# Performance work log

Hardware: AMD Instinct MI355X
Metric: run time of the kernel (lower is better)

The kernel has to match this reference:

```python
import jax, jax.numpy as jnp
import numpy as np

# ---- static config (mirrors init_kwargs + fixed setup box dims) ----
PC_MIN = jnp.array([0.0, -40.0, -3.0])
VOXEL_SIZE = jnp.array([0.05, 0.05, 0.1])
STRIDE = 4                     # pool_cfg.STRIDE and multi_scale_3d_strides['x_conv4']
EXTEND = 2.0                   # model_cfg.ROI_EXTEND_FACTOR
GRID_ZYX = (10, 400, 352)      # sparse spatial shape after stride-4 downsample [z,y,x]
# grid_size = round(extended_dims / voxel_size / STRIDE) for fixed dims [6.4,3.2,1.6]
GX, GY, GZ = 64, 32, 4
G = GX * GY * GZ
N_VOX, C = 200_000, 128
M = 64
KX, KY, KZ = 7, 7, 3


def setup_inputs() -> dict:
    key = jax.random.key(0)
    k1, k2, k3, k4, k5, k6, k7, k8, k9 = jax.random.split(key, 9)
    ctr = jnp.stack([
        jax.random.uniform(k1, (M,), minval=10.0, maxval=60.0),
        jax.random.uniform(k2, (M,), minval=-25.0, maxval=25.0),
        jax.random.uniform(k3, (M,), minval=-1.5, maxval=0.5)], axis=-1)
    dims = jnp.tile(jnp.array([[6.4, 3.2, 1.6]], jnp.float32), (M, 1))  # fixed -> static grid
    yaw = jax.random.uniform(k4, (M, 1), minval=-np.pi, maxval=np.pi)
    rois = jnp.concatenate([ctr, dims, yaw], axis=-1).astype(jnp.float32)
    proto_box = jnp.array([0.0, 0.0, 0.0, 6.4, 3.2, 1.6, 0.3], jnp.float32)
    voxel_feats = jax.random.normal(k5, (N_VOX, C), jnp.float32)
    feat_proto = jax.random.normal(k6, (1, KX, KY, KZ, C), jnp.float32) * 0.1
    zc = jax.random.randint(k7, (N_VOX,), 0, GRID_ZYX[0])
    yc = jax.random.randint(k8, (N_VOX,), 0, GRID_ZYX[1])
    xc = jax.random.randint(k9, (N_VOX,), 0, GRID_ZYX[2])
    voxel_coords = jnp.stack([jnp.zeros_like(zc), zc, yc, xc], -1).astype(jnp.int32)
    return dict(rois=rois, proto_box=proto_box, voxel_feats=voxel_feats,
                feat_proto=feat_proto, voxel_coords=voxel_coords)


def _dense_grid_points(box):
    # get_dense_grid_points: row-major (x,y,z) index order, matches torch nonzero()
    idx = jnp.stack(jnp.meshgrid(jnp.arange(GX), jnp.arange(GY), jnp.arange(GZ),
                                 indexing='ij'), -1).reshape(-1, 3).astype(jnp.float32)
    gs = jnp.array([GX, GY, GZ], jnp.float32)
    return (idx + 0.5) / gs * box[3:6] - box[3:6] / 2.0  # (G,3)


def _rotate_z(pts, ang):
    # common_utils.rotate_points_along_z: pts @ [[c,s,0],[-s,c,0],[0,0,1]]
    c, s = jnp.cos(ang), jnp.sin(ang)
    R = jnp.stack([jnp.stack([c, s, 0.0 * c]),
                   jnp.stack([-s, c, 0.0 * c]),
                   jnp.stack([0.0 * c, 0.0 * c, 1.0 + 0.0 * c])])
    return pts @ R


def reference(rois, proto_box, voxel_feats, feat_proto, voxel_coords):
    # generate_voxel2pinds: dense [Z,Y,X] grid of voxel row indices, -1 = empty
    v2p = -jnp.ones(GRID_ZYX, jnp.int32)
    v2p = v2p.at[voxel_coords[:, 1], voxel_coords[:, 2], voxel_coords[:, 3]].set(
        jnp.arange(N_VOX, dtype=jnp.int32))

    def per_roi(box):
        box = box.at[3:5].multiply(EXTEND)                 # xy_dim_extend
        local = _dense_grid_points(box)                    # (G,3)
        xyz = _rotate_z(local, box[6]) + box[:3]           # global roi grid points
        coords = jnp.floor((xyz - PC_MIN) / VOXEL_SIZE)    # '//' floor-div semantics
        coords = jnp.floor(coords / STRIDE).astype(jnp.int32)
        xc, yc, zc = coords[:, 0], coords[:, 1], coords[:, 2]
        inb = ((zc >= 0) & (zc < GRID_ZYX[0]) & (yc >= 0) & (yc < GRID_ZYX[1]) &
               (xc >= 0) & (xc < GRID_ZYX[2]))
        pidx = v2p[jnp.clip(zc, 0, GRID_ZYX[0] - 1),
                   jnp.clip(yc, 0, GRID_ZYX[1] - 1),
                   jnp.clip(xc, 0, GRID_ZYX[2] - 1)]
        valid = inb & (pidx >= 0)
        feat = jnp.where(valid[:, None], voxel_feats[jnp.clip(pidx, 0)], 0.0)  # (G,C)
        return feat, xyz

    feats, grid_xyz = jax.vmap(per_roi)(rois)              # (M,G,C), (M,G,3)
    vol = feats.reshape(M, GX, GY, GZ, C).transpose(0, 4, 1, 2, 3)   # NCDHW
    kern = feat_proto.transpose(0, 4, 1, 2, 3)                        # (1,C,KX,KY,KZ)
    pads = [(KX // 2,) * 2, (KY // 2,) * 2, (KZ // 2,) * 2]           # ceil((k-1)/2)
    mm = jax.lax.conv_general_dilated(vol, kern, (1, 1, 1), pads,
                                      dimension_numbers=('NCDHW', 'OIDHW', 'NCDHW'))
    # fresh BatchNorm3d(1) applied per-ROI (batch 1 each call): per-sample norm
    mu = jnp.mean(mm, axis=(1, 2, 3, 4), keepdims=True)
    var = jnp.var(mm, axis=(1, 2, 3, 4), keepdims=True)
    mm = (mm - mu) / jnp.sqrt(var + 1e-5)
    idx = jnp.minimum(jnp.argmax(mm.reshape(M, -1), axis=1), G - 1)
    sel = jnp.take_along_axis(grid_xyz, idx[:, None, None], axis=1)[:, 0, :]  # (M,3)
    rois_new = jnp.tile(proto_box[None], (M, 1))
    rois_new = rois_new.at[:, :3].set(sel)
    return rois_new
```

## Files before the change

### kernel.cpp

```cpp
#include <hip/hip_runtime.h>
#include <stdint.h>

#define GRID_Z 10
#define GRID_Y 400
#define GRID_X 352
#define NGRID (GRID_Z * GRID_Y * GRID_X)
#define NVOX 200000
#define CCH 128
#define MROI 64
#define GXD 64
#define GYD 32
#define GZD 4
#define GCELLS 8192
#define NTAPS 147
#define FPAD 132
#define TROWS 32

__device__ __forceinline__ void cell_xyz(const float* __restrict__ roi, int g,
                                         float& X, float& Y, float& Z) {
#pragma clang fp contract(off)
    int iz = g & 3;
    int iy = (g >> 2) & 31;
    int ix = g >> 7;
    float bx = roi[3] * 2.0f;
    float by = roi[4] * 2.0f;
    float bz = roi[5];
    float lx = (ix + 0.5f) / 64.0f * bx - bx / 2.0f;
    float ly = (iy + 0.5f) / 32.0f * by - by / 2.0f;
    float lz = (iz + 0.5f) / 4.0f  * bz - bz / 2.0f;
    float c = cosf(roi[6]);
    float s = sinf(roi[6]);
    X = lx * c + ly * (-s) + roi[0];
    Y = lx * s + ly * c    + roi[1];
    Z = lz + roi[2];
}

__global__ void k_scatter(const int* __restrict__ vcoords, int* __restrict__ v2p,
                          int* __restrict__ cnt) {
    int i = blockIdx.x * 256 + threadIdx.x;
    if (blockIdx.x == 0 && threadIdx.x < MROI) cnt[threadIdx.x] = 0;
    if (i >= NVOX) return;
    int z = vcoords[i * 4 + 1];
    int y = vcoords[i * 4 + 2];
    int x = vcoords[i * 4 + 3];
    atomicMax(&v2p[(z * GRID_Y + y) * GRID_X + x], i);
}

__global__ void k_build(const float* __restrict__ rois, const int* __restrict__ v2p,
                        unsigned* __restrict__ list, int* __restrict__ cnt) {
#pragma clang fp contract(off)
    int g = blockIdx.x * 256 + threadIdx.x;
    int m = blockIdx.y;
    int lane = threadIdx.x & 63;
    const float* roi = rois + m * 7;
    float X, Y, Z;
    cell_xyz(roi, g, X, Y, Z);
    float fx = floorf((X - 0.0f)     / 0.05f);
    float fy = floorf((Y - (-40.0f)) / 0.05f);
    float fz = floorf((Z - (-3.0f))  / 0.1f);
    int cx = (int)floorf(fx / 4.0f);
    int cy = (int)floorf(fy / 4.0f);
    int cz = (int)floorf(fz / 4.0f);
    int p = -1;
    if (cz >= 0 && cz < GRID_Z && cy >= 0 && cy < GRID_Y && cx >= 0 && cx < GRID_X)
        p = v2p[(cz * GRID_Y + cy) * GRID_X + cx];
    bool v = p >= 0;
    unsigned long long bal = __ballot(v);
    int nset = __popcll(bal);
    int base = 0;
    if (lane == 0 && nset) base = atomicAdd(&cnt[m], nset);
    base = __shfl(base, 0, 64);
    if (v) {
        int pos = __popcll(bal & ((1ull << lane) - 1ull));
        list[m * GCELLS + base + pos] = ((unsigned)p << 13) | (unsigned)g;
    }
}

__global__ __launch_bounds__(256) void k_dots(
        const float* __restrict__ vfeat, const float* __restrict__ fproto,
        const unsigned* __restrict__ list, const int* __restrict__ cnt,
        float* __restrict__ partial) {
    __shared__ float    sscore[GCELLS];
    __shared__ float    sfeat[TROWS * FPAD];
    __shared__ unsigned sg[TROWS];

    const int m    = blockIdx.y;
    const int NS   = gridDim.x;
    const int tid  = threadIdx.x;
    const int w    = tid >> 6;
    const int lane = tid & 63;
    const int vi   = lane & 7;
    const int ti   = (lane >> 3) & 7;
    const int n    = cnt[m];
    const unsigned* lst = list + m * GCELLS;
    const int tbase = w * 40 + ti;

    int tkx[5], tky[5], tkz[5], tok[5];
    #pragma unroll
    for (int b = 0; b < 5; ++b) {
        int t = tbase + 8 * b;
        tok[b] = t < NTAPS;
        int tc = tok[b] ? t : (NTAPS - 1);
        int kx  = tc / 21;
        int rem = tc - kx * 21;
        tkx[b] = kx;
        tky[b] = rem / 3;
        tkz[b] = rem - tky[b] * 3;
    }

    {
        float4* s4 = (float4*)sscore;
        #pragma unroll
        for (int i = 0; i < GCELLS / 4 / 256; ++i)
            s4[tid + 256 * i] = make_float4(0.f, 0.f, 0.f, 0.f);
    }

    for (int vt0 = blockIdx.x * TROWS; vt0 < n; vt0 += TROWS * NS) {
        __syncthreads();
        {
            int r = tid >> 3;
            int q = tid & 7;
            int v = vt0 + r;
            unsigned e = 0xFFFFFFFFu;
            if (v < n) e = lst[v];
            if (q == 0) sg[r] = e;
            if (e != 0xFFFFFFFFu) {
                int p = (int)(e >> 13);
                const float4* src = (const float4*)(vfeat + (size_t)p * CCH) + q * 4;
                float4* drow = (float4*)(sfeat + r * FPAD + q * 16);
                #pragma unroll
                for (int j = 0; j < 4; ++j) drow[j] = src[j];
            }
        }
        __syncthreads();

        float acc[4][5];
        #pragma unroll
        for (int a = 0; a < 4; ++a)
            #pragma unroll
            for (int b = 0; b < 5; ++b) acc[a][b] = 0.0f;

        #pragma unroll 1
        for (int k = 0; k < CCH; k += 4) {
            float4 f[4];
            #pragma unroll
            for (int a = 0; a < 4; ++a)
                f[a] = *(const float4*)&sfeat[(vi + 8 * a) * FPAD + k];
            float4 wv[5];
            #pragma unroll
            for (int b = 0; b < 5; ++b)
                wv[b] = *(const float4*)(fproto + (tbase + (tok[b] ? 8 * b : 0)) * CCH + k);
            #pragma unroll
            for (int a = 0; a < 4; ++a)
                #pragma unroll
                for (int b = 0; b < 5; ++b) {
                    acc[a][b] = fmaf(f[a].x, wv[b].x, acc[a][b]);
                    acc[a][b] = fmaf(f[a].y, wv[b].y, acc[a][b]);
                    acc[a][b] = fmaf(f[a].z, wv[b].z, acc[a][b]);
                    acc[a][b] = fmaf(f[a].w, wv[b].w, acc[a][b]);
                }
        }

        #pragma unroll
        for (int b = 0; b < 5; ++b) {
            if (!tok[b]) continue;
            #pragma unroll
            for (int a = 0; a < 4; ++a) {
                unsigned e = sg[vi + 8 * a];
                if (e == 0xFFFFFFFFu) continue;
                int g  = (int)(e & 8191u);
                int cx = (g >> 7)        - (tkx[b] - 3);
                int cy = ((g >> 2) & 31) - (tky[b] - 3);
                int cz = (g & 3)         - (tkz[b] - 1);
                if ((unsigned)cx < (unsigned)GXD && (unsigned)cy < (unsigned)GYD &&
                    (unsigned)cz < (unsigned)GZD)
                    atomicAdd(&sscore[(cx << 7) | (cy << 2) | cz], acc[a][b]);
            }
        }
    }

    __syncthreads();
    {
        float* dst = partial + ((size_t)m * NS + blockIdx.x) * GCELLS;
        const float4* s4 = (const float4*)sscore;
        float4* d4 = (float4*)dst;
        #pragma unroll
        for (int i = 0; i < GCELLS / 4 / 256; ++i)
            d4[tid + 256 * i] = s4[tid + 256 * i];
    }
}

template <int NS>
__global__ __launch_bounds__(1024) void k_argfin(
        const float* __restrict__ partial,
        const float* __restrict__ rois,
        const float* __restrict__ pbox,
        float* __restrict__ out) {
    __shared__ unsigned long long red[1024];
    int m = blockIdx.x;
    int tid = threadIdx.x;
    const float* base = partial + (size_t)m * NS * GCELLS;
    unsigned long long bk = 0ull;
    #pragma unroll
    for (int i = 0; i < GCELLS / 1024; ++i) {
        int g = tid + 1024 * i;
        float v = 0.0f;
        #pragma unroll
        for (int s = 0; s < NS; ++s) v += base[s * GCELLS + g];
        unsigned ub  = __float_as_uint(v);
        unsigned key = (ub & 0x80000000u) ? ~ub : (ub | 0x80000000u);
        unsigned long long pk =
            ((unsigned long long)key << 32) | (unsigned)(GCELLS - 1 - g);
        bk = bk > pk ? bk : pk;
    }
    red[tid] = bk;
    __syncthreads();
    for (int s = 512; s > 0; s >>= 1) {
        if (tid < s) {
            unsigned long long o = red[tid + s];
            if (o > red[tid]) red[tid] = o;
        }
        __syncthreads();
    }
    if (tid == 0) {
        int g = (GCELLS - 1) - (int)(unsigned)(red[0] & 0xFFFFFFFFu);
        float X, Y, Z;
        cell_xyz(rois + m * 7, g, X, Y, Z);
        out[m * 7 + 0] = X;
        out[m * 7 + 1] = Y;
        out[m * 7 + 2] = Z;
        out[m * 7 + 3] = pbox[3];
        out[m * 7 + 4] = pbox[4];
        out[m * 7 + 5] = pbox[5];
        out[m * 7 + 6] = pbox[6];
    }
}

extern "C" void kernel_launch(void* const* d_in, const int* in_sizes, int n_in,
                              void* d_out, int out_size, void* d_ws, size_t ws_size,
                              hipStream_t stream) {
    const float* rois    = (const float*)d_in[0];
    const float* pbox    = (const float*)d_in[1];
    const float* vfeat   = (const float*)d_in[2];
    const float* fproto  = (const float*)d_in[3];
    const int*   vcoords = (const int*)d_in[4];
    float* out = (float*)d_out;

    int*      v2p  = (int*)d_ws;
    unsigned* list = (unsigned*)(v2p + NGRID);
    int*      cnt  = (int*)(list + MROI * GCELLS);
    size_t    base = ((size_t)NGRID + (size_t)MROI * GCELLS) * 4 + 256;
    int NS; float* partial;
    if (ws_size >= base + (size_t)12 * MROI * GCELLS * 4) {
        NS = 12; partial = (float*)((char*)d_ws + base);
    } else if (ws_size >= base + (size_t)8 * MROI * GCELLS * 4) {
        NS = 8;  partial = (float*)((char*)d_ws + base);
    } else if (ws_size >= base + (size_t)4 * MROI * GCELLS * 4) {
        NS = 4;  partial = (float*)((char*)d_ws + base);
    } else {
        NS = 2;  partial = (float*)v2p;
    }

    hipMemsetAsync(v2p, 0xFF, (size_t)NGRID * 4, stream);
    k_scatter<<<(NVOX + 255) / 256, 256, 0, stream>>>(vcoords, v2p, cnt);
    k_build  <<<dim3(GCELLS / 256, MROI), 256, 0, stream>>>(rois, v2p, list, cnt);
    k_dots   <<<dim3(NS, MROI), 256, 0, stream>>>(vfeat, fproto, list, cnt, partial);
    if (NS == 12)      k_argfin<12><<<MROI, 1024, 0, stream>>>(partial, rois, pbox, out);
    else if (NS == 8)  k_argfin<8> <<<MROI, 1024, 0, stream>>>(partial, rois, pbox, out);
    else if (NS == 4)  k_argfin<4> <<<MROI, 1024, 0, stream>>>(partial, rois, pbox, out);
    else               k_argfin<2> <<<MROI, 1024, 0, stream>>>(partial, rois, pbox, out);
}
```

Baseline: 300.5 us.

## Fuse pipeline into one cooperative kernel with grid syncs

Replaces the memset plus four separate kernel launches with a single cooperative kernel that runs the v2p reset, scatter, list build, dot-product scoring and argmax phases, separated by grid-wide barriers. The argmax is split across all 768 blocks, each reducing a chunk and combining through a 64-bit atomicMax. The aim is to remove launch gaps and the tail of the small argmax kernel. In exchange, the phases now cost grid.sync overhead, and the 768 blocks must all be resident (the code requires at least 3 blocks per CU, each using about 49KB of shared memory). If the occupancy check or the cooperative launch fails, it falls back to the old multi-kernel path.

```diff
diff --git a/kernel.cpp b/kernel.cpp
--- a/kernel.cpp
+++ b/kernel.cpp
@@ -1,5 +1,8 @@
 #include <hip/hip_runtime.h>
+#include <hip/hip_cooperative_groups.h>
 #include <stdint.h>
+
+namespace cg = cooperative_groups;
 
 #define GRID_Z 10
 #define GRID_Y 400
@@ -15,6 +18,10 @@
 #define NTAPS 147
 #define FPAD 132
 #define TROWS 32
+#define NS12 12
+#define NBLK (NS12 * MROI)
+#define NTH  (NBLK * 256)
+#define CHUNK ((GCELLS + NS12 - 1) / NS12)
 
 __device__ __forceinline__ void cell_xyz(const float* __restrict__ roi, int g,
                                          float& X, float& Y, float& Z) {
@@ -35,24 +42,9 @@
     Z = lz + roi[2];
 }
 
-__global__ void k_scatter(const int* __restrict__ vcoords, int* __restrict__ v2p,
-                          int* __restrict__ cnt) {
-    int i = blockIdx.x * 256 + threadIdx.x;
-    if (blockIdx.x == 0 && threadIdx.x < MROI) cnt[threadIdx.x] = 0;
-    if (i >= NVOX) return;
-    int z = vcoords[i * 4 + 1];
-    int y = vcoords[i * 4 + 2];
-    int x = vcoords[i * 4 + 3];
-    atomicMax(&v2p[(z * GRID_Y + y) * GRID_X + x], i);
-}
-
-__global__ void k_build(const float* __restrict__ rois, const int* __restrict__ v2p,
-                        unsigned* __restrict__ list, int* __restrict__ cnt) {
+__device__ __forceinline__ int cell_to_pidx(const float* __restrict__ roi, int g,
+                                            const int* __restrict__ v2p) {
 #pragma clang fp contract(off)
-    int g = blockIdx.x * 256 + threadIdx.x;
-    int m = blockIdx.y;
-    int lane = threadIdx.x & 63;
-    const float* roi = rois + m * 7;
     float X, Y, Z;
     cell_xyz(roi, g, X, Y, Z);
     float fx = floorf((X - 0.0f)     / 0.05f);
@@ -64,6 +56,224 @@
     int p = -1;
     if (cz >= 0 && cz < GRID_Z && cy >= 0 && cy < GRID_Y && cx >= 0 && cx < GRID_X)
         p = v2p[(cz * GRID_Y + cy) * GRID_X + cx];
+    return p;
+}
+
+__global__ __launch_bounds__(256) void k_mega(
+        const float* __restrict__ rois, const float* __restrict__ pbox,
+        const float* __restrict__ vfeat, const float* __restrict__ fproto,
+        const int* __restrict__ vcoords,
+        int* __restrict__ v2p, unsigned* __restrict__ list, int* __restrict__ cnt,
+        float* __restrict__ partial, unsigned long long* __restrict__ best,
+        float* __restrict__ out) {
+    __shared__ float    sscore[GCELLS];
+    __shared__ float    sfeat[TROWS * FPAD];
+    __shared__ unsigned sg[TROWS];
+
+    cg::grid_group grid = cg::this_grid();
+    const int tid  = threadIdx.x;
+    const int gtid = blockIdx.x * 256 + tid;
+    const int lane = tid & 63;
+
+    for (int i = gtid; i < NGRID; i += NTH) v2p[i] = -1;
+    if (gtid < MROI) { cnt[gtid] = 0; best[gtid] = 0ull; }
+    grid.sync();
+
+    for (int i = gtid; i < NVOX; i += NTH) {
+        int z = vcoords[i * 4 + 1];
+        int y = vcoords[i * 4 + 2];
+        int x = vcoords[i * 4 + 3];
+        atomicMax(&v2p[(z * GRID_Y + y) * GRID_X + x], i);
+    }
+    grid.sync();
+
+    for (int idx = gtid; idx < MROI * GCELLS; idx += NTH) {
+        int m = idx >> 13;
+        int g = idx & 8191;
+        int p = cell_to_pidx(rois + m * 7, g, v2p);
+        bool v = p >= 0;
+        unsigned long long bal = __ballot(v);
+        int nset = __popcll(bal);
+        int base = 0;
+        if (lane == 0 && nset) base = atomicAdd(&cnt[m], nset);
+        base = __shfl(base, 0, 64);
+        if (v) {
+            int pos = __popcll(bal & ((1ull << lane) - 1ull));
+            list[m * GCELLS + base + pos] = ((unsigned)p << 13) | (unsigned)g;
+        }
+    }
+    grid.sync();
+
+    {
+        const int m = blockIdx.x & 63;
+        const int s = blockIdx.x >> 6;
+        const int w    = tid >> 6;
+        const int vi   = lane & 7;
+        const int ti   = (lane >> 3) & 7;
+        const int n    = cnt[m];
+        const unsigned* lst = list + m * GCELLS;
+        const int tbase = w * 40 + ti;
+
+        int tkx[5], tky[5], tkz[5], tok[5];
+        #pragma unroll
+        for (int b = 0; b < 5; ++b) {
+            int t = tbase + 8 * b;
+            tok[b] = t < NTAPS;
+            int tc = tok[b] ? t : (NTAPS - 1);
+            int kx  = tc / 21;
+            int rem = tc - kx * 21;
+            tkx[b] = kx;
+            tky[b] = rem / 3;
+            tkz[b] = rem - tky[b] * 3;
+        }
+
+        {
+            float4* s4 = (float4*)sscore;
+            #pragma unroll
+            for (int i = 0; i < GCELLS / 4 / 256; ++i)
+                s4[tid + 256 * i] = make_float4(0.f, 0.f, 0.f, 0.f);
+        }
+
+        for (int vt0 = s * TROWS; vt0 < n; vt0 += TROWS * NS12) {
+            __syncthreads();
+            {
+                int r = tid >> 3;
+                int q = tid & 7;
+                int v = vt0 + r;
+                unsigned e = 0xFFFFFFFFu;
+                if (v < n) e = lst[v];
+                if (q == 0) sg[r] = e;
+                if (e != 0xFFFFFFFFu) {
+                    int p = (int)(e >> 13);
+                    const float4* src = (const float4*)(vfeat + (size_t)p * CCH) + q * 4;
+                    float4* drow = (float4*)(sfeat + r * FPAD + q * 16);
+                    #pragma unroll
+                    for (int j = 0; j < 4; ++j) drow[j] = src[j];
+                }
+            }
+            __syncthreads();
+
+            float acc[4][5];
+            #pragma unroll
+            for (int a = 0; a < 4; ++a)
+                #pragma unroll
+                for (int b = 0; b < 5; ++b) acc[a][b] = 0.0f;
+
+            #pragma unroll 1
+            for (int k = 0; k < CCH; k += 4) {
+                float4 f[4];
+                #pragma unroll
+                for (int a = 0; a < 4; ++a)
+                    f[a] = *(const float4*)&sfeat[(vi + 8 * a) * FPAD + k];
+                float4 wv[5];
+                #pragma unroll
+                for (int b = 0; b < 5; ++b)
+                    wv[b] = *(const float4*)(fproto + (tbase + (tok[b] ? 8 * b : 0)) * CCH + k);
+                #pragma unroll
+                for (int a = 0; a < 4; ++a)
+                    #pragma unroll
+                    for (int b = 0; b < 5; ++b) {
+                        acc[a][b] = fmaf(f[a].x, wv[b].x, acc[a][b]);
+                        acc[a][b] = fmaf(f[a].y, wv[b].y, acc[a][b]);
+                        acc[a][b] = fmaf(f[a].z, wv[b].z, acc[a][b]);
+                        acc[a][b] = fmaf(f[a].w, wv[b].w, acc[a][b]);
+                    }
+            }
+
+            #pragma unroll
+            for (int b = 0; b < 5; ++b) {
+                if (!tok[b]) continue;
+                #pragma unroll
+                for (int a = 0; a < 4; ++a) {
+                    unsigned e = sg[vi + 8 * a];
+                    if (e == 0xFFFFFFFFu) continue;
+                    int g  = (int)(e & 8191u);
+                    int cx = (g >> 7)        - (tkx[b] - 3);
+                    int cy = ((g >> 2) & 31) - (tky[b] - 3);
+                    int cz = (g & 3)         - (tkz[b] - 1);
+                    if ((unsigned)cx < (unsigned)GXD && (unsigned)cy < (unsigned)GYD &&
+                        (unsigned)cz < (unsigned)GZD)
+                        atomicAdd(&sscore[(cx << 7) | (cy << 2) | cz], acc[a][b]);
+                }
+            }
+        }
+
+        __syncthreads();
+        {
+            float* dst = partial + ((size_t)m * NS12 + s) * GCELLS;
+            const float4* s4 = (const float4*)sscore;
+            float4* d4 = (float4*)dst;
+            #pragma unroll
+            for (int i = 0; i < GCELLS / 4 / 256; ++i)
+                d4[tid + 256 * i] = s4[tid + 256 * i];
+        }
+    }
+    grid.sync();
+
+    {
+        int m = blockIdx.x & 63;
+        int s = blockIdx.x >> 6;
+        const float* basep = partial + (size_t)m * NS12 * GCELLS;
+        int c0 = s * CHUNK;
+        int c1 = c0 + CHUNK < GCELLS ? c0 + CHUNK : GCELLS;
+        unsigned long long bk = 0ull;
+        for (int c = c0 + tid; c < c1; c += 256) {
+            float v = 0.0f;
+            #pragma unroll
+            for (int q = 0; q < NS12; ++q) v += basep[q * GCELLS + c];
+            unsigned ub  = __float_as_uint(v);
+            unsigned key = (ub & 0x80000000u) ? ~ub : (ub | 0x80000000u);
+            unsigned long long pk =
+                ((unsigned long long)key << 32) | (unsigned)(GCELLS - 1 - c);
+            bk = bk > pk ? bk : pk;
+        }
+        __syncthreads();
+        unsigned long long* red = reinterpret_cast<unsigned long long*>(sscore);
+        red[tid] = bk;
+        __syncthreads();
+        for (int st = 128; st > 0; st >>= 1) {
+            if (tid < st) {
+                unsigned long long o = red[tid + st];
+                if (o > red[tid]) red[tid] = o;
+            }
+            __syncthreads();
+        }
+        if (tid == 0) atomicMax(&best[m], red[0]);
+    }
+    grid.sync();
+
+    if (blockIdx.x == 0 && tid < MROI) {
+        int m = tid;
+        int g = (GCELLS - 1) - (int)(unsigned)(best[m] & 0xFFFFFFFFu);
+        float X, Y, Z;
+        cell_xyz(rois + m * 7, g, X, Y, Z);
+        out[m * 7 + 0] = X;
+        out[m * 7 + 1] = Y;
+        out[m * 7 + 2] = Z;
+        out[m * 7 + 3] = pbox[3];
+        out[m * 7 + 4] = pbox[4];
+        out[m * 7 + 5] = pbox[5];
+        out[m * 7 + 6] = pbox[6];
+    }
+}
+
+__global__ void k_scatter(const int* __restrict__ vcoords, int* __restrict__ v2p,
+                          int* __restrict__ cnt) {
+    int i = blockIdx.x * 256 + threadIdx.x;
+    if (blockIdx.x == 0 && threadIdx.x < MROI) cnt[threadIdx.x] = 0;
+    if (i >= NVOX) return;
+    int z = vcoords[i * 4 + 1];
+    int y = vcoords[i * 4 + 2];
+    int x = vcoords[i * 4 + 3];
+    atomicMax(&v2p[(z * GRID_Y + y) * GRID_X + x], i);
+}
+
+__global__ void k_build(const float* __restrict__ rois, const int* __restrict__ v2p,
+                        unsigned* __restrict__ list, int* __restrict__ cnt) {
+    int g = blockIdx.x * 256 + threadIdx.x;
+    int m = blockIdx.y;
+    int lane = threadIdx.x & 63;
+    int p = cell_to_pidx(rois + m * 7, g, v2p);
     bool v = p >= 0;
     unsigned long long bal = __ballot(v);
     int nset = __popcll(bal);
@@ -85,7 +295,7 @@
     __shared__ unsigned sg[TROWS];
 
     const int m    = blockIdx.y;
-    const int NS   = gridDim.x;
+    const int NSd  = gridDim.x;
     const int tid  = threadIdx.x;
     const int w    = tid >> 6;
     const int lane = tid & 63;
@@ -103,24 +313,18 @@
         int tc = tok[b] ? t : (NTAPS - 1);
         int kx  = tc / 21;
         int rem = tc - kx * 21;
-        tkx[b] = kx;
-        tky[b] = rem / 3;
-        tkz[b] = rem - tky[b] * 3;
-    }
-
+        tkx[b] = kx; tky[b] = rem / 3; tkz[b] = rem - tky[b] * 3;
+    }
     {
         float4* s4 = (float4*)sscore;
         #pragma unroll
         for (int i = 0; i < GCELLS / 4 / 256; ++i)
             s4[tid + 256 * i] = make_float4(0.f, 0.f, 0.f, 0.f);
     }
-
-    for (int vt0 = blockIdx.x * TROWS; vt0 < n; vt0 += TROWS * NS) {
+    for (int vt0 = blockIdx.x * TROWS; vt0 < n; vt0 += TROWS * NSd) {
         __syncthreads();
         {
-            int r = tid >> 3;
-            int q = tid & 7;
-            int v = vt0 + r;
+            int r = tid >> 3, q = tid & 7, v = vt0 + r;
             unsigned e = 0xFFFFFFFFu;
             if (v < n) e = lst[v];
             if (q == 0) sg[r] = e;
@@ -133,13 +337,11 @@
             }
         }
         __syncthreads();
-
         float acc[4][5];
         #pragma unroll
         for (int a = 0; a < 4; ++a)
             #pragma unroll
             for (int b = 0; b < 5; ++b) acc[a][b] = 0.0f;
-
         #pragma unroll 1
         for (int k = 0; k < CCH; k += 4) {
             float4 f[4];
@@ -160,7 +362,6 @@
                     acc[a][b] = fmaf(f[a].w, wv[b].w, acc[a][b]);
                 }
         }
-
         #pragma unroll
         for (int b = 0; b < 5; ++b) {
             if (!tok[b]) continue;
@@ -178,10 +379,9 @@
             }
         }
     }
-
     __syncthreads();
     {
-        float* dst = partial + ((size_t)m * NS + blockIdx.x) * GCELLS;
+        float* dst = partial + ((size_t)m * NSd + blockIdx.x) * GCELLS;
         const float4* s4 = (const float4*)sscore;
         float4* d4 = (float4*)dst;
         #pragma unroll
@@ -192,10 +392,8 @@
 
 template <int NS>
 __global__ __launch_bounds__(1024) void k_argfin(
-        const float* __restrict__ partial,
-        const float* __restrict__ rois,
-        const float* __restrict__ pbox,
-        float* __restrict__ out) {
+        const float* __restrict__ partial, const float* __restrict__ rois,
+        const float* __restrict__ pbox, float* __restrict__ out) {
     __shared__ unsigned long long red[1024];
     int m = blockIdx.x;
     int tid = threadIdx.x;
@@ -249,24 +447,39 @@
     int*      v2p  = (int*)d_ws;
     unsigned* list = (unsigned*)(v2p + NGRID);
     int*      cnt  = (int*)(list + MROI * GCELLS);
-    size_t    base = ((size_t)NGRID + (size_t)MROI * GCELLS) * 4 + 256;
-    int NS; float* partial;
+    float*    partial = (float*)((char*)cnt + 256);
+    unsigned long long* best =
+        (unsigned long long*)(partial + (size_t)NS12 * MROI * GCELLS);
+    size_t need = (size_t)((char*)(best + MROI) - (char*)d_ws);
+
+    int maxb = 0;
+    hipError_t oe = hipOccupancyMaxActiveBlocksPerMultiprocessor(&maxb, k_mega, 256, 0);
+    if (oe == hipSuccess && maxb >= 3 && ws_size >= need) {
+        void* args[] = { (void*)&rois, (void*)&pbox, (void*)&vfeat, (void*)&fproto,
+                         (void*)&vcoords, (void*)&v2p, (void*)&list, (void*)&cnt,
+                         (void*)&partial, (void*)&best, (void*)&out };
+        hipError_t e = hipLaunchCooperativeKernel((const void*)k_mega, dim3(NBLK),
+                                                  dim3(256), args, 0, stream);
+        if (e == hipSuccess) return;
+    }
+
+    size_t base = ((size_t)NGRID + (size_t)MROI * GCELLS) * 4 + 256;
+    int NS; float* fpartial;
     if (ws_size >= base + (size_t)12 * MROI * GCELLS * 4) {
-        NS = 12; partial = (float*)((char*)d_ws + base);
+        NS = 12; fpartial = (float*)((char*)d_ws + base);
     } else if (ws_size >= base + (size_t)8 * MROI * GCELLS * 4) {
-        NS = 8;  partial = (float*)((char*)d_ws + base);
+        NS = 8;  fpartial = (float*)((char*)d_ws + base);
     } else if (ws_size >= base + (size_t)4 * MROI * GCELLS * 4) {
-        NS = 4;  partial = (float*)((char*)d_ws + base);
+        NS = 4;  fpartial = (float*)((char*)d_ws + base);
     } else {
-        NS = 2;  partial = (float*)v2p;
-    }
-
+        NS = 2;  fpartial = (float*)v2p;
+    }
     hipMemsetAsync(v2p, 0xFF, (size_t)NGRID * 4, stream);
     k_scatter<<<(NVOX + 255) / 256, 256, 0, stream>>>(vcoords, v2p, cnt);
     k_build  <<<dim3(GCELLS / 256, MROI), 256, 0, stream>>>(rois, v2p, list, cnt);
-    k_dots   <<<dim3(NS, MROI), 256, 0, stream>>>(vfeat, fproto, list, cnt, partial);
-    if (NS == 12)      k_argfin<12><<<MROI, 1024, 0, stream>>>(partial, rois, pbox, out);
-    else if (NS == 8)  k_argfin<8> <<<MROI, 1024, 0, stream>>>(partial, rois, pbox, out);
-    else if (NS == 4)  k_argfin<4> <<<MROI, 1024, 0, stream>>>(partial, rois, pbox, out);
-    else               k_argfin<2> <<<MROI, 1024, 0, stream>>>(partial, rois, pbox, out);
-}
+    k_dots   <<<dim3(NS, MROI), 256, 0, stream>>>(vfeat, fproto, list, cnt, fpartial);
+    if (NS == 12)      k_argfin<12><<<MROI, 1024, 0, stream>>>(fpartial, rois, pbox, out);
+    else if (NS == 8)  k_argfin<8> <<<MROI, 1024, 0, stream>>>(fpartial, rois, pbox, out);
+    else if (NS == 4)  k_argfin<4> <<<MROI, 1024, 0, stream>>>(fpartial, rois, pbox, out);
+    else               k_argfin<2> <<<MROI, 1024, 0, stream>>>(fpartial, rois, pbox, out);
+}
```

Result: no change. 299.6 us (-0.3%).

## Fuse list build, dot products and argmax into one kernel with last-block finish

Applied to the files above, without the earlier changes.

Merges the per-ROI occupied-cell list build, the tap dot-product scatter and the final argmax into a single kernel. Each block builds its own slice of the cell list in shared memory, so there is no global list and no global counter. The last block to finish for each ROI, detected through an atomic done counter, reduces the partial score grids and writes the output. This removes two kernel launches and the global list round trip, at the cost of a fixed-capacity shared list (CAP) that could overflow if a slice has more occupied cells than expected. It also adds threadfence-based cross-block synchronisation.

```diff
diff --git a/kernel.cpp b/kernel.cpp
--- a/kernel.cpp
+++ b/kernel.cpp
@@ -35,26 +35,20 @@
     Z = lz + roi[2];
 }
 
-__global__ void k_scatter(const int* __restrict__ vcoords, int* __restrict__ v2p,
-                          int* __restrict__ cnt) {
-    int i = blockIdx.x * 256 + threadIdx.x;
-    if (blockIdx.x == 0 && threadIdx.x < MROI) cnt[threadIdx.x] = 0;
-    if (i >= NVOX) return;
-    int z = vcoords[i * 4 + 1];
-    int y = vcoords[i * 4 + 2];
-    int x = vcoords[i * 4 + 3];
-    atomicMax(&v2p[(z * GRID_Y + y) * GRID_X + x], i);
-}
-
-__global__ void k_build(const float* __restrict__ rois, const int* __restrict__ v2p,
-                        unsigned* __restrict__ list, int* __restrict__ cnt) {
+__device__ __forceinline__ int cell_probe(float bx, float by, float bz,
+                                          float cs, float sn,
+                                          float ox, float oy, float oz,
+                                          int g, const int* __restrict__ v2p) {
 #pragma clang fp contract(off)
-    int g = blockIdx.x * 256 + threadIdx.x;
-    int m = blockIdx.y;
-    int lane = threadIdx.x & 63;
-    const float* roi = rois + m * 7;
-    float X, Y, Z;
-    cell_xyz(roi, g, X, Y, Z);
+    int iz = g & 3;
+    int iy = (g >> 2) & 31;
+    int ix = g >> 7;
+    float lx = (ix + 0.5f) / 64.0f * bx - bx / 2.0f;
+    float ly = (iy + 0.5f) / 32.0f * by - by / 2.0f;
+    float lz = (iz + 0.5f) / 4.0f  * bz - bz / 2.0f;
+    float X = lx * cs + ly * (-sn) + ox;
+    float Y = lx * sn + ly * cs    + oy;
+    float Z = lz + oz;
     float fx = floorf((X - 0.0f)     / 0.05f);
     float fy = floorf((Y - (-40.0f)) / 0.05f);
     float fz = floorf((Z - (-3.0f))  / 0.1f);
@@ -64,160 +58,194 @@
     int p = -1;
     if (cz >= 0 && cz < GRID_Z && cy >= 0 && cy < GRID_Y && cx >= 0 && cx < GRID_X)
         p = v2p[(cz * GRID_Y + cy) * GRID_X + cx];
-    bool v = p >= 0;
-    unsigned long long bal = __ballot(v);
-    int nset = __popcll(bal);
-    int base = 0;
-    if (lane == 0 && nset) base = atomicAdd(&cnt[m], nset);
-    base = __shfl(base, 0, 64);
-    if (v) {
-        int pos = __popcll(bal & ((1ull << lane) - 1ull));
-        list[m * GCELLS + base + pos] = ((unsigned)p << 13) | (unsigned)g;
-    }
-}
-
-__global__ __launch_bounds__(256) void k_dots(
+    return p;
+}
+
+__global__ void k_scatter(const int* __restrict__ vcoords, int* __restrict__ v2p,
+                          int* __restrict__ done) {
+    int i = blockIdx.x * 256 + threadIdx.x;
+    if (blockIdx.x == 0 && threadIdx.x < MROI) done[threadIdx.x] = 0;
+    if (i >= NVOX) return;
+    int z = vcoords[i * 4 + 1];
+    int y = vcoords[i * 4 + 2];
+    int x = vcoords[i * 4 + 3];
+    atomicMax(&v2p[(z * GRID_Y + y) * GRID_X + x], i);
+}
+
+template <int NS, int CAP>
+__global__ __launch_bounds__(256) void k_fused(
+        const float* __restrict__ rois, const float* __restrict__ pbox,
         const float* __restrict__ vfeat, const float* __restrict__ fproto,
-        const unsigned* __restrict__ list, const int* __restrict__ cnt,
-        float* __restrict__ partial) {
+        const int* __restrict__ v2p, float* __restrict__ partial,
+        int* __restrict__ done, float* __restrict__ out) {
     __shared__ float    sscore[GCELLS];
     __shared__ float    sfeat[TROWS * FPAD];
     __shared__ unsigned sg[TROWS];
-
-    const int m    = blockIdx.y;
-    const int NS   = gridDim.x;
+    __shared__ unsigned llist[CAP];
+    __shared__ int      lcnt;
+    __shared__ int      slast;
+
+    const int m    = blockIdx.x & 63;
+    const int s    = blockIdx.x >> 6;
     const int tid  = threadIdx.x;
     const int w    = tid >> 6;
     const int lane = tid & 63;
-    const int vi   = lane & 7;
-    const int ti   = (lane >> 3) & 7;
-    const int n    = cnt[m];
-    const unsigned* lst = list + m * GCELLS;
-    const int tbase = w * 40 + ti;
-
-    int tkx[5], tky[5], tkz[5], tok[5];
-    #pragma unroll
-    for (int b = 0; b < 5; ++b) {
-        int t = tbase + 8 * b;
-        tok[b] = t < NTAPS;
-        int tc = tok[b] ? t : (NTAPS - 1);
-        int kx  = tc / 21;
-        int rem = tc - kx * 21;
-        tkx[b] = kx;
-        tky[b] = rem / 3;
-        tkz[b] = rem - tky[b] * 3;
-    }
-
+    const float* roi = rois + m * 7;
+
+    if (tid == 0) lcnt = 0;
     {
         float4* s4 = (float4*)sscore;
         #pragma unroll
         for (int i = 0; i < GCELLS / 4 / 256; ++i)
             s4[tid + 256 * i] = make_float4(0.f, 0.f, 0.f, 0.f);
     }
-
-    for (int vt0 = blockIdx.x * TROWS; vt0 < n; vt0 += TROWS * NS) {
-        __syncthreads();
+    __syncthreads();
+
+    {
+        float bx, by, bz, cs, sn, ox, oy, oz;
         {
-            int r = tid >> 3;
-            int q = tid & 7;
-            int v = vt0 + r;
-            unsigned e = 0xFFFFFFFFu;
-            if (v < n) e = lst[v];
-            if (q == 0) sg[r] = e;
-            if (e != 0xFFFFFFFFu) {
-                int p = (int)(e >> 13);
-                const float4* src = (const float4*)(vfeat + (size_t)p * CCH) + q * 4;
-                float4* drow = (float4*)(sfeat + r * FPAD + q * 16);
-                #pragma unroll
-                for (int j = 0; j < 4; ++j) drow[j] = src[j];
-            }
-        }
-        __syncthreads();
-
-        float acc[4][5];
-        #pragma unroll
-        for (int a = 0; a < 4; ++a)
-            #pragma unroll
-            for (int b = 0; b < 5; ++b) acc[a][b] = 0.0f;
-
-        #pragma unroll 1
-        for (int k = 0; k < CCH; k += 4) {
-            float4 f[4];
+#pragma clang fp contract(off)
+            bx = roi[3] * 2.0f; by = roi[4] * 2.0f; bz = roi[5];
+            cs = cosf(roi[6]);  sn = sinf(roi[6]);
+            ox = roi[0]; oy = roi[1]; oz = roi[2];
+        }
+        for (int j = w; s + NS * j < GCELLS / 64; j += 4) {
+            int g = (s + NS * j) * 64 + lane;
+            int p = cell_probe(bx, by, bz, cs, sn, ox, oy, oz, g, v2p);
+            bool v = p >= 0;
+            unsigned long long bal = __ballot(v);
+            int nset = __popcll(bal);
+            int base = 0;
+            if (lane == 0 && nset) base = atomicAdd(&lcnt, nset);
+            base = __shfl(base, 0, 64);
+            if (v) {
+                int pos = __popcll(bal & ((1ull << lane) - 1ull));
+                llist[base + pos] = ((unsigned)p << 13) | (unsigned)g;
+            }
+        }
+    }
+    __syncthreads();
+    const int n = lcnt;
+
+    {
+        const int vi = lane & 7;
+        const int ti = (lane >> 3) & 7;
+        const int tbase = w * 40 + ti;
+
+        int tkx[5], tky[5], tkz[5], tok[5];
+        #pragma unroll
+        for (int b = 0; b < 5; ++b) {
+            int t = tbase + 8 * b;
+            tok[b] = t < NTAPS;
+            int tc = tok[b] ? t : (NTAPS - 1);
+            int kx  = tc / 21;
+            int rem = tc - kx * 21;
+            tkx[b] = kx;
+            tky[b] = rem / 3;
+            tkz[b] = rem - tky[b] * 3;
+        }
+
+        for (int vt0 = 0; vt0 < n; vt0 += TROWS) {
+            __syncthreads();
+            {
+                int r = tid >> 3;
+                int q = tid & 7;
+                int v = vt0 + r;
+                unsigned e = 0xFFFFFFFFu;
+                if (v < n) e = llist[v];
+                if (q == 0) sg[r] = e;
+                if (e != 0xFFFFFFFFu) {
+                    int p = (int)(e >> 13);
+                    const float4* src = (const float4*)(vfeat + (size_t)p * CCH) + q * 4;
+                    float4* drow = (float4*)(sfeat + r * FPAD + q * 16);
+                    #pragma unroll
+                    for (int j = 0; j < 4; ++j) drow[j] = src[j];
+                }
+            }
+            __syncthreads();
+
+            float acc[4][5];
             #pragma unroll
             for (int a = 0; a < 4; ++a)
-                f[a] = *(const float4*)&sfeat[(vi + 8 * a) * FPAD + k];
-            float4 wv[5];
+                #pragma unroll
+                for (int b = 0; b < 5; ++b) acc[a][b] = 0.0f;
+
+            #pragma unroll 1
+            for (int k = 0; k < CCH; k += 4) {
+                float4 f[4];
+                #pragma unroll
+                for (int a = 0; a < 4; ++a)
+                    f[a] = *(const float4*)&sfeat[(vi + 8 * a) * FPAD + k];
+                float4 wv[5];
+                #pragma unroll
+                for (int b = 0; b < 5; ++b)
+                    wv[b] = *(const float4*)(fproto + (tbase + (tok[b] ? 8 * b : 0)) * CCH + k);
+                #pragma unroll
+                for (int a = 0; a < 4; ++a)
+                    #pragma unroll
+                    for (int b = 0; b < 5; ++b) {
+                        acc[a][b] = fmaf(f[a].x, wv[b].x, acc[a][b]);
+                        acc[a][b] = fmaf(f[a].y, wv[b].y, acc[a][b]);
+                        acc[a][b] = fmaf(f[a].z, wv[b].z, acc[a][b]);
+                        acc[a][b] = fmaf(f[a].w, wv[b].w, acc[a][b]);
+                    }
+            }
+
             #pragma unroll
-            for (int b = 0; b < 5; ++b)
-                wv[b] = *(const float4*)(fproto + (tbase + (tok[b] ? 8 * b : 0)) * CCH + k);
-            #pragma unroll
-            for (int a = 0; a < 4; ++a)
-                #pragma unroll
-                for (int b = 0; b < 5; ++b) {
-                    acc[a][b] = fmaf(f[a].x, wv[b].x, acc[a][b]);
-                    acc[a][b] = fmaf(f[a].y, wv[b].y, acc[a][b]);
-                    acc[a][b] = fmaf(f[a].z, wv[b].z, acc[a][b]);
-                    acc[a][b] = fmaf(f[a].w, wv[b].w, acc[a][b]);
+            for (int b = 0; b < 5; ++b) {
+                if (!tok[b]) continue;
+                #pragma unroll
+                for (int a = 0; a < 4; ++a) {
+                    unsigned e = sg[vi + 8 * a];
+                    if (e == 0xFFFFFFFFu) continue;
+                    int g  = (int)(e & 8191u);
+                    int cx = (g >> 7)        - (tkx[b] - 3);
+                    int cy = ((g >> 2) & 31) - (tky[b] - 3);
+                    int cz = (g & 3)         - (tkz[b] - 1);
+                    if ((unsigned)cx < (unsigned)GXD && (unsigned)cy < (unsigned)GYD &&
+                        (unsigned)cz < (unsigned)GZD)
+                        atomicAdd(&sscore[(cx << 7) | (cy << 2) | cz], acc[a][b]);
                 }
-        }
-
-        #pragma unroll
-        for (int b = 0; b < 5; ++b) {
-            if (!tok[b]) continue;
-            #pragma unroll
-            for (int a = 0; a < 4; ++a) {
-                unsigned e = sg[vi + 8 * a];
-                if (e == 0xFFFFFFFFu) continue;
-                int g  = (int)(e & 8191u);
-                int cx = (g >> 7)        - (tkx[b] - 3);
-                int cy = ((g >> 2) & 31) - (tky[b] - 3);
-                int cz = (g & 3)         - (tkz[b] - 1);
-                if ((unsigned)cx < (unsigned)GXD && (unsigned)cy < (unsigned)GYD &&
-                    (unsigned)cz < (unsigned)GZD)
-                    atomicAdd(&sscore[(cx << 7) | (cy << 2) | cz], acc[a][b]);
-            }
-        }
-    }
-
-    __syncthreads();
-    {
-        float* dst = partial + ((size_t)m * NS + blockIdx.x) * GCELLS;
+            }
+        }
+    }
+
+    __syncthreads();
+    {
+        float* dst = partial + ((size_t)m * NS + s) * GCELLS;
         const float4* s4 = (const float4*)sscore;
         float4* d4 = (float4*)dst;
         #pragma unroll
         for (int i = 0; i < GCELLS / 4 / 256; ++i)
             d4[tid + 256 * i] = s4[tid + 256 * i];
     }
-}
-
-template <int NS>
-__global__ __launch_bounds__(1024) void k_argfin(
-        const float* __restrict__ partial,
-        const float* __restrict__ rois,
-        const float* __restrict__ pbox,
-        float* __restrict__ out) {
-    __shared__ unsigned long long red[1024];
-    int m = blockIdx.x;
-    int tid = threadIdx.x;
-    const float* base = partial + (size_t)m * NS * GCELLS;
+    __threadfence();
+    __syncthreads();
+    if (tid == 0) slast = (atomicAdd(&done[m], 1) == NS - 1) ? 1 : 0;
+    __syncthreads();
+    if (!slast) return;
+    __threadfence();
+
+    const float* basep = partial + (size_t)m * NS * GCELLS;
     unsigned long long bk = 0ull;
-    #pragma unroll
-    for (int i = 0; i < GCELLS / 1024; ++i) {
-        int g = tid + 1024 * i;
+    #pragma unroll 1
+    for (int i = 0; i < GCELLS / 256; ++i) {
+        int g = tid + 256 * i;
         float v = 0.0f;
         #pragma unroll
-        for (int s = 0; s < NS; ++s) v += base[s * GCELLS + g];
+        for (int q = 0; q < NS; ++q) v += basep[q * GCELLS + g];
         unsigned ub  = __float_as_uint(v);
         unsigned key = (ub & 0x80000000u) ? ~ub : (ub | 0x80000000u);
         unsigned long long pk =
             ((unsigned long long)key << 32) | (unsigned)(GCELLS - 1 - g);
         bk = bk > pk ? bk : pk;
     }
+    unsigned long long* red = reinterpret_cast<unsigned long long*>(sscore);
     red[tid] = bk;
     __syncthreads();
-    for (int s = 512; s > 0; s >>= 1) {
-        if (tid < s) {
-            unsigned long long o = red[tid + s];
+    for (int st = 128; st > 0; st >>= 1) {
+        if (tid < st) {
+            unsigned long long o = red[tid + st];
             if (o > red[tid]) red[tid] = o;
         }
         __syncthreads();
@@ -225,7 +253,7 @@
     if (tid == 0) {
         int g = (GCELLS - 1) - (int)(unsigned)(red[0] & 0xFFFFFFFFu);
         float X, Y, Z;
-        cell_xyz(rois + m * 7, g, X, Y, Z);
+        cell_xyz(roi, g, X, Y, Z);
         out[m * 7 + 0] = X;
         out[m * 7 + 1] = Y;
         out[m * 7 + 2] = Z;
@@ -246,27 +274,24 @@
     const int*   vcoords = (const int*)d_in[4];
     float* out = (float*)d_out;
 
-    int*      v2p  = (int*)d_ws;
-    unsigned* list = (unsigned*)(v2p + NGRID);
-    int*      cnt  = (int*)(list + MROI * GCELLS);
-    size_t    base = ((size_t)NGRID + (size_t)MROI * GCELLS) * 4 + 256;
-    int NS; float* partial;
-    if (ws_size >= base + (size_t)12 * MROI * GCELLS * 4) {
-        NS = 12; partial = (float*)((char*)d_ws + base);
-    } else if (ws_size >= base + (size_t)8 * MROI * GCELLS * 4) {
-        NS = 8;  partial = (float*)((char*)d_ws + base);
-    } else if (ws_size >= base + (size_t)4 * MROI * GCELLS * 4) {
-        NS = 4;  partial = (float*)((char*)d_ws + base);
+    int*   v2p = (int*)d_ws;
+    float* partial = (float*)(v2p + NGRID);
+
+    size_t need12 = (size_t)NGRID * 4 + (size_t)12 * MROI * GCELLS * 4 + 256;
+    size_t need4  = (size_t)NGRID * 4 + (size_t)4  * MROI * GCELLS * 4 + 256;
+
+    hipMemsetAsync(v2p, 0xFF, (size_t)NGRID * 4, stream);
+
+    if (ws_size >= need12) {
+        int* done = (int*)(partial + (size_t)12 * MROI * GCELLS);
+        k_scatter<<<(NVOX + 255) / 256, 256, 0, stream>>>(vcoords, v2p, done);
+        k_fused<12, 704><<<12 * MROI, 256, 0, stream>>>(
+            rois, pbox, vfeat, fproto, v2p, partial, done, out);
     } else {
-        NS = 2;  partial = (float*)v2p;
-    }
-
-    hipMemsetAsync(v2p, 0xFF, (size_t)NGRID * 4, stream);
-    k_scatter<<<(NVOX + 255) / 256, 256, 0, stream>>>(vcoords, v2p, cnt);
-    k_build  <<<dim3(GCELLS / 256, MROI), 256, 0, stream>>>(rois, v2p, list, cnt);
-    k_dots   <<<dim3(NS, MROI), 256, 0, stream>>>(vfeat, fproto, list, cnt, partial);
-    if (NS == 12)      k_argfin<12><<<MROI, 1024, 0, stream>>>(partial, rois, pbox, out);
-    else if (NS == 8)  k_argfin<8> <<<MROI, 1024, 0, stream>>>(partial, rois, pbox, out);
-    else if (NS == 4)  k_argfin<4> <<<MROI, 1024, 0, stream>>>(partial, rois, pbox, out);
-    else               k_argfin<2> <<<MROI, 1024, 0, stream>>>(partial, rois, pbox, out);
-}
+        int* done = (int*)(partial + (size_t)4 * MROI * GCELLS);
+        (void)need4;
+        k_scatter<<<(NVOX + 255) / 256, 256, 0, stream>>>(vcoords, v2p, done);
+        k_fused<4, 2048><<<4 * MROI, 256, 0, stream>>>(
+            rois, pbox, vfeat, fproto, v2p, partial, done, out);
+    }
+}
```

Measured after the change: 340.4 us. 13.3% more time.
